# Kernel optimization log

Hardware: AMD Instinct MI355X
Metric: run time of the kernel (lower is better)

## Reference

```python
import jax, jax.numpy as jnp
import numpy as np

D_MODEL = 1024
D_STATE = 16
D_CONV = 3
EXPAND = 2
D_INNER = EXPAND * D_MODEL
BATCH = 1
SEQ = 2048


def _xavier(key, fan_in, fan_out, shape):
    lim = float(np.sqrt(6.0 / (fan_in + fan_out)))
    return jax.random.uniform(key, shape, jnp.float32, -lim, lim)


def setup_inputs() -> dict:
    key = jax.random.key(0)
    ks = jax.random.split(key, 8)
    return {
        "x": jax.random.normal(ks[0], (BATCH, SEQ, D_MODEL), jnp.float32),
        # torch Linear weight (out,in) stored transposed as (in,out) for x @ W
        "in_proj_w": _xavier(ks[1], D_MODEL, 2 * D_INNER, (D_MODEL, 2 * D_INNER)),
        "in_proj_b": jnp.zeros((2 * D_INNER,), jnp.float32),
        "conv_w": _xavier(ks[2], D_MODEL * D_CONV, D_INNER, (D_INNER, D_MODEL, D_CONV)),
        "conv_b": jax.random.normal(ks[3], (D_INNER,), jnp.float32) * 0.02,
        # A_log shifted negative so softplus(A_log) is tiny and the (unstable-by-construction)
        # recurrence with A_bar=exp(+A*dt)>1 stays finite over SEQ steps
        "A_log": jax.random.normal(ks[4], (D_INNER, D_STATE), jnp.float32) * 0.1 - 6.0,
        "D": jnp.ones((D_INNER,), jnp.float32),
        "x_proj_w": _xavier(ks[5], D_INNER, 2 * D_STATE, (D_INNER, 2 * D_STATE)),
        "x_proj_b": jnp.zeros((2 * D_STATE,), jnp.float32),
        "gate_w": _xavier(ks[6], D_INNER, D_INNER, (D_INNER, D_INNER)),
        "gate_b": jnp.zeros((D_INNER,), jnp.float32),
        "o_proj_w": _xavier(ks[7], D_INNER, D_MODEL, (D_INNER, D_MODEL)),
        "o_proj_b": jnp.zeros((D_MODEL,), jnp.float32),
    }


def _forward(x, in_proj_w, in_proj_b, conv_w, conv_b, A_log, D, x_proj_w, x_proj_b,
             gate_w, gate_b, o_proj_w, o_proj_b):
    B, S, _ = x.shape
    # causal depthful conv: torch pads both sides by d_conv-1 then truncates to S,
    # which equals left-pad-only by d_conv-1
    xc = jax.lax.conv_general_dilated(
        x.transpose(0, 2, 1), conv_w, (1,), [(D_CONV - 1, 0)],
        dimension_numbers=("NCH", "OIH", "NCH"))
    x_conv = xc.transpose(0, 2, 1) + conv_b            # (B,S,d_inner)

    xz = x @ in_proj_w + in_proj_b                      # (B,S,2*d_inner)
    z = xz[..., D_INNER:]                               # gate branch (x_inner unused)

    A = jax.nn.softplus(A_log)                          # (d_inner,d_state)
    bc = x_conv @ x_proj_w + x_proj_b                   # (B,S,2*d_state)
    Bm, Cm = bc[..., :D_STATE], bc[..., D_STATE:]
    dt = jax.nn.sigmoid(jnp.mean(x_conv, axis=-1, keepdims=True)) + 0.001  # (B,S,1)
    gate = jax.nn.sigmoid(x_conv @ gate_w + gate_b)
    u = x_conv * gate                                   # (B,S,d_inner)

    dtE = dt[..., None]                                 # (B,S,1,1)
    A_bar = jnp.exp(A[None, None] * dtE)                # (B,S,d_inner,d_state)
    B_bar = A_bar * Bm[:, :, None, :] * dtE             # (B,S,d_inner,d_state)

    def step(h, inp):
        ab, bb, ut, ct = inp                            # (B,di,ds),(B,di,ds),(B,di),(B,ds)
        h = ab * h + bb * ut[:, :, None]
        y = jnp.einsum("bds,bs->bd", h, ct) + D * ut
        return h, y

    h0 = jnp.zeros((B, D_INNER, D_STATE), x.dtype)
    _, ys = jax.lax.scan(
        step, h0,
        (A_bar.transpose(1, 0, 2, 3), B_bar.transpose(1, 0, 2, 3),
         u.transpose(1, 0, 2), Cm.transpose(1, 0, 2)))
    out = ys.transpose(1, 0, 2) * jax.nn.sigmoid(z)     # (B,S,d_inner)
    return out @ o_proj_w + o_proj_b                    # (B,S,d_model)


def reference(x, in_proj_w, in_proj_b, conv_w, conv_b, A_log, D, x_proj_w, x_proj_b,
              gate_w, gate_b, o_proj_w, o_proj_b):
    return _forward(x, in_proj_w, in_proj_b, conv_w, conv_b, A_log, D,
                    x_proj_w, x_proj_b, gate_w, gate_b, o_proj_w, o_proj_b)
```

## Files before the change

kernel.cpp:

```cpp
#include <hip/hip_runtime.h>
#include <hip/hip_bf16.h>
#include <math.h>

typedef __attribute__((ext_vector_type(8))) short short8;
typedef __attribute__((ext_vector_type(4))) float f32x4;

#define NCH 128
#define CT 16

__device__ __forceinline__ unsigned short f2bf(float f) {
  unsigned u = __builtin_bit_cast(unsigned, f);
  u += 0x7fffu + ((u >> 16) & 1u);
  return (unsigned short)(u >> 16);
}
__device__ __forceinline__ float bf2f(unsigned short u) {
  return __builtin_bit_cast(float, (unsigned)u << 16);
}
__device__ __forceinline__ float sigm(float x) { return 1.f / (1.f + __expf(-x)); }
__device__ __forceinline__ float exps(float x) {
  return 1.f + x * (1.f + x * (0.5f + x * 0.16666667f));
}

__device__ __forceinline__ void stage16(const void* g, void* l) {
  __builtin_amdgcn_global_load_lds(
      (const __attribute__((address_space(1))) unsigned int*)(unsigned long long)g,
      (__attribute__((address_space(3))) unsigned int*)(unsigned)(unsigned long long)l,
      16, 0, 0);
}

__global__ __launch_bounds__(256) void prep_uber(
    const float* __restrict__ x, const float* __restrict__ conv_w,
    const float* __restrict__ A_log, const float* __restrict__ in_proj_w,
    const float* __restrict__ gate_w, const float* __restrict__ o_proj_w,
    unsigned short* __restrict__ xb, unsigned short* __restrict__ cwt,
    float* __restrict__ cAb, unsigned short* __restrict__ wzt,
    unsigned short* __restrict__ gwt, unsigned short* __restrict__ owt) {
  __shared__ float tile[32][33];
  int bx = blockIdx.x;
  if (bx < 2050) {
    int idx = (bx * 256 + threadIdx.x) * 4;
    if (idx >= 2050 * 1024) return;
    int row = idx >> 10, col = idx & 1023;
    float v0 = 0.f, v1 = 0.f, v2 = 0.f, v3 = 0.f;
    if (row >= 2) {
      const float4 v = *(const float4*)(x + (size_t)(row - 2) * 1024 + col);
      v0 = v.x; v1 = v.y; v2 = v.z; v3 = v.w;
    }
    unsigned long long pk = (unsigned long long)f2bf(v0)
        | ((unsigned long long)f2bf(v1) << 16)
        | ((unsigned long long)f2bf(v2) << 32)
        | ((unsigned long long)f2bf(v3) << 48);
    *(unsigned long long*)(xb + idx) = pk;
    return;
  }
  bx -= 2050;
  if (bx < 8192) {
    int idx = bx * 256 + threadIdx.x;
    int d = idx >> 10, i = idx & 1023;
    const float* p = conv_w + (size_t)d * 3072 + (size_t)i * 3;
    unsigned short* q = cwt + (size_t)d * 3072 + i;
    q[0] = f2bf(p[0]);
    q[1024] = f2bf(p[1]);
    q[2048] = f2bf(p[2]);
    return;
  }
  bx -= 8192;
  if (bx < 128) {
    int i = bx * 256 + threadIdx.x;
    cAb[i] = log1pf(__expf(A_log[i]));
    return;
  }
  bx -= 128;
  const float* W;
  unsigned short* Wt;
  int src_ld, col_off, rowsI, n0, i0;
  if (bx < 2048) {
    W = in_proj_w; Wt = wzt; src_ld = 4096; col_off = 2048; rowsI = 1024;
    n0 = (bx & 63) * 32; i0 = (bx >> 6) * 32;
  } else if (bx < 2048 + 4096) {
    int b = bx - 2048;
    W = gate_w; Wt = gwt; src_ld = 2048; col_off = 0; rowsI = 2048;
    n0 = (b & 63) * 32; i0 = (b >> 6) * 32;
  } else {
    int b = bx - 2048 - 4096;
    W = o_proj_w; Wt = owt; src_ld = 1024; col_off = 0; rowsI = 2048;
    n0 = (b & 31) * 32; i0 = (b >> 5) * 32;
  }
  int tx = threadIdx.x & 31, ty = threadIdx.x >> 5;
#pragma unroll
  for (int rr = 0; rr < 32; rr += 8)
    tile[ty + rr][tx] = W[(size_t)(i0 + ty + rr) * src_ld + col_off + n0 + tx];
  __syncthreads();
#pragma unroll
  for (int rr = 0; rr < 32; rr += 8)
    Wt[(size_t)(n0 + ty + rr) * rowsI + i0 + tx] = f2bf(tile[tx][ty + rr]);
}

template <int MODE>
__device__ __forceinline__ void gemm_sq_body(
    const unsigned short* __restrict__ A, int lda,
    const unsigned short* __restrict__ Bt, int ldb, int K,
    const float* __restrict__ bias,
    float* __restrict__ outf, int ldo,
    unsigned short* __restrict__ outb,
    int bm, int bn,
    unsigned short (*As)[128 * 64], unsigned short (*Bs)[128 * 64]) {
  const int tid = threadIdx.x;
  const int lane = tid & 63;
  const int w = tid >> 6;
  const int wr = w >> 1, wc = w & 1;

  f32x4 acc[4][4];
#pragma unroll
  for (int m = 0; m < 4; ++m)
#pragma unroll
    for (int n = 0; n < 4; ++n)
#pragma unroll
      for (int j = 0; j < 4; ++j) acc[m][n][j] = 0.f;

  const int srow = lane >> 3;
  const int sslot = (lane & 7) ^ srow;
  const unsigned short* Ab = A + (size_t)(bm * 128 + srow) * lda + sslot * 8;
  const unsigned short* Bb = Bt + (size_t)(bn * 128 + srow) * ldb + sslot * 8;

  const int r = lane & 15;
  const int g = lane >> 4;
  const int nk = K >> 6;

  auto stage = [&](int buf, int k0) {
#pragma unroll
    for (int i = 0; i < 4; ++i) {
      const int cb = w * 4 + i;
      stage16(Ab + (size_t)(cb * 8) * lda + k0, &As[buf][cb * 512]);
    }
#pragma unroll
    for (int i = 0; i < 4; ++i) {
      const int cb = w * 4 + i;
      stage16(Bb + (size_t)(cb * 8) * ldb + k0, &Bs[buf][cb * 512]);
    }
  };

  auto compute = [&](int buf) {
#pragma unroll
    for (int kk = 0; kk < 64; kk += 32) {
      const int sb = (kk >> 3) + g;
      short8 af[4], bfr[4];
#pragma unroll
      for (int m = 0; m < 4; ++m) {
        const int R = wr * 64 + m * 16 + r;
        af[m] = *(const short8*)&As[buf][R * 64 + ((sb ^ (R & 7)) << 3)];
      }
#pragma unroll
      for (int n = 0; n < 4; ++n) {
        const int R = wc * 64 + n * 16 + r;
        bfr[n] = *(const short8*)&Bs[buf][R * 64 + ((sb ^ (R & 7)) << 3)];
      }
#pragma unroll
      for (int m = 0; m < 4; ++m)
#pragma unroll
        for (int n = 0; n < 4; ++n)
          acc[m][n] = __builtin_amdgcn_mfma_f32_16x16x32_bf16(af[m], bfr[n], acc[m][n], 0, 0, 0);
    }
  };

  stage(0, 0);
  int cur = 0;
  for (int kt = 0; kt < nk; ++kt) {
    if (kt + 1 < nk) {
      stage(cur ^ 1, (kt + 1) * 64);
      asm volatile("s_waitcnt vmcnt(8)" ::: "memory");
    } else {
      asm volatile("s_waitcnt vmcnt(0)" ::: "memory");
    }
    __builtin_amdgcn_s_barrier();
    __builtin_amdgcn_sched_barrier(0);
    compute(cur);
    __builtin_amdgcn_s_barrier();
    cur ^= 1;
  }

  const int cc = lane & 15;
  const int cr = g * 4;
#pragma unroll
  for (int m = 0; m < 4; ++m) {
#pragma unroll
    for (int n = 0; n < 4; ++n) {
      const int col = bn * 128 + wc * 64 + n * 16 + cc;
      const float bv = bias[col];
#pragma unroll
      for (int j = 0; j < 4; ++j) {
        const int row = bm * 128 + wr * 64 + m * 16 + cr + j;
        const size_t o = (size_t)row * ldo + col;
        float v = acc[m][n][j] + bv;
        if (MODE == 0) { outb[o] = f2bf(v); }
        else if (MODE == 1) { outf[o] = v; }
        else { outb[o] = f2bf(sigm(v)); }
      }
    }
  }
}

__global__ __launch_bounds__(256, 2) void gemm_convz(
    const unsigned short* __restrict__ xb,
    const unsigned short* __restrict__ cwt,
    const unsigned short* __restrict__ wzt,
    const float* __restrict__ conv_b,
    const float* __restrict__ z_b,
    unsigned short* __restrict__ xcb,
    unsigned short* __restrict__ zpre_b) {
  __shared__ unsigned short As[2][128 * 64];
  __shared__ unsigned short Bs[2][128 * 64];
  const bool isz = blockIdx.y >= 16;
  gemm_sq_body<0>(isz ? xb + 2048 : xb, 1024,
                  isz ? wzt : cwt, isz ? 1024 : 3072, isz ? 1024 : 3072,
                  isz ? z_b : conv_b, nullptr, 2048,
                  isz ? zpre_b : xcb,
                  blockIdx.x, isz ? blockIdx.y - 16 : blockIdx.y, As, Bs);
}

#define RB 4
__global__ __launch_bounds__(256, 2) void gemm_gate64_bcdt(
    const unsigned short* __restrict__ xcb,
    const unsigned short* __restrict__ gwt,
    const float* __restrict__ gate_b,
    unsigned short* __restrict__ gpre_b,
    const float* __restrict__ xpw, const float* __restrict__ xpb,
    float* __restrict__ Bc, float* __restrict__ Cc, float* __restrict__ dt) {
  constexpr int L = 4;
  __shared__ __attribute__((aligned(16))) char smem[49152];
  unsigned short (*As)[4096] = (unsigned short(*)[4096])smem;
  unsigned short (*Bs)[4096] = (unsigned short(*)[4096])(smem + 24576);
  const int tid = threadIdx.x;
  const int lane = tid & 63;
  const int w = tid >> 6;

  if (blockIdx.y >= 32) {
    float (*row)[2048] = (float(*)[2048])smem;
    float (*pj)[8][32] = (float(*)[8][32])(smem + 32768);
    const int b = (blockIdx.y - 32) * 32 + blockIdx.x;
    const int s0 = b * RB;
    for (int i = tid; i < RB * 256; i += 256) {
      int ri = i >> 8, c8 = i & 255;
      short8 v = *(const short8*)&xcb[(size_t)(s0 + ri) * 2048 + c8 * 8];
#pragma unroll
      for (int j = 0; j < 8; ++j) row[ri][c8 * 8 + j] = bf2f((unsigned short)v[j]);
    }
    __syncthreads();
    {
      float l = 0.f;
      for (int i = lane; i < 2048; i += 64) l += row[w][i];
#pragma unroll
      for (int off = 32; off > 0; off >>= 1) l += __shfl_down(l, off);
      if (lane == 0) dt[s0 + w] = sigm(l * (1.f / 2048.f)) + 0.001f;
    }
    const int j = tid & 31, seg = tid >> 5;
    float acc[RB] = {0.f, 0.f, 0.f, 0.f};
    const int kbase = seg * 256;
    for (int k = 0; k < 256; ++k) {
      float wv2 = xpw[(size_t)(kbase + k) * 32 + j];
#pragma unroll
      for (int ri = 0; ri < RB; ++ri) acc[ri] += row[ri][kbase + k] * wv2;
    }
#pragma unroll
    for (int ri = 0; ri < RB; ++ri) pj[ri][seg][j] = acc[ri];
    __syncthreads();
    if (tid < 32 * RB) {
      int ri = tid >> 5, jj = tid & 31;
      float v = xpb[jj];
#pragma unroll
      for (int q = 0; q < 8; ++q) v += pj[ri][q][jj];
      if (jj < 16) Bc[(size_t)(s0 + ri) * 16 + jj] = v;
      else Cc[(size_t)(s0 + ri) * 16 + jj - 16] = v;
    }
    return;
  }

  const int wr = w >> 1, wc = w & 1;
  const int bm = blockIdx.x, bn = blockIdx.y;

  f32x4 acc[2][2];
#pragma unroll
  for (int m = 0; m < 2; ++m)
#pragma unroll
    for (int n = 0; n < 2; ++n)
#pragma unroll
      for (int j = 0; j < 4; ++j) acc[m][n][j] = 0.f;

  const int srow = lane >> 3;
  const int sslot = (lane & 7) ^ srow;
  const unsigned short* Ab = xcb + (size_t)(bm * 64 + srow) * 2048 + sslot * 8;
  const unsigned short* Bb = gwt + (size_t)(bn * 64 + srow) * 2048 + sslot * 8;
  const int r = lane & 15;
  const int g = lane >> 4;
  const int nk = 2048 >> 6;

  auto stage = [&](int buf, int k0) {
#pragma unroll
    for (int i = 0; i < 2; ++i) {
      const int cb = w * 2 + i;
      stage16(Ab + (size_t)(cb * 8) * 2048 + k0, &As[buf][cb * 512]);
      stage16(Bb + (size_t)(cb * 8) * 2048 + k0, &Bs[buf][cb * 512]);
    }
  };
  auto compute = [&](int buf) {
#pragma unroll
    for (int kk = 0; kk < 64; kk += 32) {
      const int sb = (kk >> 3) + g;
      short8 af[2], bfr[2];
#pragma unroll
      for (int m = 0; m < 2; ++m) {
        const int R = wr * 32 + m * 16 + r;
        af[m] = *(const short8*)&As[buf][R * 64 + ((sb ^ (R & 7)) << 3)];
      }
#pragma unroll
      for (int n = 0; n < 2; ++n) {
        const int R = wc * 32 + n * 16 + r;
        bfr[n] = *(const short8*)&Bs[buf][R * 64 + ((sb ^ (R & 7)) << 3)];
      }
#pragma unroll
      for (int m = 0; m < 2; ++m)
#pragma unroll
        for (int n = 0; n < 2; ++n)
          acc[m][n] = __builtin_amdgcn_mfma_f32_16x16x32_bf16(af[m], bfr[n], acc[m][n], 0, 0, 0);
    }
  };

  stage(0, 0);
  stage(1, 64);
  int cur = 0, nxt = 2;
  for (int kt = 0; kt < nk; ++kt) {
    if (kt + 2 < nk) {
      stage(nxt, (kt + 2) * 64);
      asm volatile("s_waitcnt vmcnt(%c0)" ::"i"(2 * L) : "memory");
    } else if (kt + 1 < nk) {
      asm volatile("s_waitcnt vmcnt(%c0)" ::"i"(L) : "memory");
    } else {
      asm volatile("s_waitcnt vmcnt(0)" ::: "memory");
    }
    __builtin_amdgcn_s_barrier();
    __builtin_amdgcn_sched_barrier(0);
    compute(cur);
    __builtin_amdgcn_s_barrier();
    cur = (cur == 2) ? 0 : cur + 1;
    nxt = (nxt == 2) ? 0 : nxt + 1;
  }

  const int cc = lane & 15;
  const int cr = g * 4;
#pragma unroll
  for (int m = 0; m < 2; ++m)
#pragma unroll
    for (int n = 0; n < 2; ++n) {
      const int col = bn * 64 + wc * 32 + n * 16 + cc;
      const float bv = gate_b[col];
#pragma unroll
      for (int j = 0; j < 4; ++j) {
        const int row = bm * 64 + wr * 32 + m * 16 + cr + j;
        gpre_b[(size_t)row * 2048 + col] = f2bf(sigm(acc[m][n][j] + bv));
      }
    }
}

__global__ __launch_bounds__(256, 2) void gemm_out(
    const unsigned short* __restrict__ A, int lda,
    const unsigned short* __restrict__ Bt, int ldb, int K,
    const float* __restrict__ bias,
    float* __restrict__ outf, int ldo) {
  constexpr int L = 4;
  __shared__ unsigned short As[3][64 * 64];
  __shared__ unsigned short Bs[3][64 * 64];
  const int tid = threadIdx.x;
  const int lane = tid & 63;
  const int w = tid >> 6;
  const int wr = w >> 1, wc = w & 1;
  const int bm = blockIdx.x, bn = blockIdx.y;

  f32x4 acc[2][2];
#pragma unroll
  for (int m = 0; m < 2; ++m)
#pragma unroll
    for (int n = 0; n < 2; ++n)
#pragma unroll
      for (int j = 0; j < 4; ++j) acc[m][n][j] = 0.f;

  const int srow = lane >> 3;
  const int sslot = (lane & 7) ^ srow;
  const unsigned short* Ab = A + (size_t)(bm * 64 + srow) * lda + sslot * 8;
  const unsigned short* Bb = Bt + (size_t)(bn * 64 + srow) * ldb + sslot * 8;
  const int r = lane & 15;
  const int g = lane >> 4;
  const int nk = K >> 6;

  auto stage = [&](int buf, int k0) {
#pragma unroll
    for (int i = 0; i < 2; ++i) {
      const int cb = w * 2 + i;
      stage16(Ab + (size_t)(cb * 8) * lda + k0, &As[buf][cb * 512]);
      stage16(Bb + (size_t)(cb * 8) * ldb + k0, &Bs[buf][cb * 512]);
    }
  };
  auto compute = [&](int buf) {
#pragma unroll
    for (int kk = 0; kk < 64; kk += 32) {
      const int sb = (kk >> 3) + g;
      short8 af[2], bfr[2];
#pragma unroll
      for (int m = 0; m < 2; ++m) {
        const int R = wr * 32 + m * 16 + r;
        af[m] = *(const short8*)&As[buf][R * 64 + ((sb ^ (R & 7)) << 3)];
      }
#pragma unroll
      for (int n = 0; n < 2; ++n) {
        const int R = wc * 32 + n * 16 + r;
        bfr[n] = *(const short8*)&Bs[buf][R * 64 + ((sb ^ (R & 7)) << 3)];
      }
#pragma unroll
      for (int m = 0; m < 2; ++m)
#pragma unroll
        for (int n = 0; n < 2; ++n)
          acc[m][n] = __builtin_amdgcn_mfma_f32_16x16x32_bf16(af[m], bfr[n], acc[m][n], 0, 0, 0);
    }
  };

  stage(0, 0);
  stage(1, 64);
  int cur = 0, nxt = 2;
  for (int kt = 0; kt < nk; ++kt) {
    if (kt + 2 < nk) {
      stage(nxt, (kt + 2) * 64);
      asm volatile("s_waitcnt vmcnt(%c0)" ::"i"(2 * L) : "memory");
    } else if (kt + 1 < nk) {
      asm volatile("s_waitcnt vmcnt(%c0)" ::"i"(L) : "memory");
    } else {
      asm volatile("s_waitcnt vmcnt(0)" ::: "memory");
    }
    __builtin_amdgcn_s_barrier();
    __builtin_amdgcn_sched_barrier(0);
    compute(cur);
    __builtin_amdgcn_s_barrier();
    cur = (cur == 2) ? 0 : cur + 1;
    nxt = (nxt == 2) ? 0 : nxt + 1;
  }

  const int cc = lane & 15;
  const int cr = g * 4;
#pragma unroll
  for (int m = 0; m < 2; ++m)
#pragma unroll
    for (int n = 0; n < 2; ++n) {
      const int col = bn * 64 + wc * 32 + n * 16 + cc;
      const float bv = bias[col];
#pragma unroll
      for (int j = 0; j < 4; ++j) {
        const int row = bm * 64 + wr * 32 + m * 16 + cr + j;
        outf[(size_t)row * ldo + col] = acc[m][n][j] + bv;
      }
    }
}

__global__ __launch_bounds__(256) void scan_local(const float* __restrict__ cAb,
                                                  const float* __restrict__ dt,
                                                  const float* __restrict__ Bc,
                                                  const float* __restrict__ Cc,
                                                  const unsigned short* __restrict__ xcb,
                                                  const unsigned short* __restrict__ gpre,
                                                  const float* __restrict__ Dp,
                                                  unsigned short* __restrict__ yloc,
                                                  unsigned short* __restrict__ Hend) {
  const int d0 = blockIdx.x * 256;
  const int d = d0 + threadIdx.x;
  const int c = blockIdx.y;
  __shared__ float sU[CT][256];
  __shared__ float sB[CT][16], sC[CT][16], sdt[CT];
  for (int i = threadIdx.x; i < CT * 32; i += 256) {
    int t = i >> 5, c8 = i & 31;
    size_t base = (size_t)(c * CT + t) * 2048 + d0 + c8 * 8;
    short8 vx = *(const short8*)&xcb[base];
    short8 vg = *(const short8*)&gpre[base];
#pragma unroll
    for (int j = 0; j < 8; ++j)
      sU[t][c8 * 8 + j] = bf2f((unsigned short)vx[j]) * bf2f((unsigned short)vg[j]);
  }
  for (int i = threadIdx.x; i < CT * 16; i += 256) {
    sB[i >> 4][i & 15] = Bc[(size_t)c * CT * 16 + i];
    sC[i >> 4][i & 15] = Cc[(size_t)c * CT * 16 + i];
  }
  if (threadIdx.x < CT) sdt[threadIdx.x] = dt[c * CT + threadIdx.x];
  __syncthreads();
  float cA[16], h[16];
#pragma unroll
  for (int n = 0; n < 16; ++n) {
    cA[n] = cAb[(size_t)d * 16 + n];
    h[n] = 0.f;
  }
  const float Dv = Dp[d];
  for (int t = 0; t < CT; ++t) {
    const float dtv = sdt[t];
    const float uv = sU[t][threadIdx.x];
    const float du = dtv * uv;
    float y = Dv * uv;
#pragma unroll
    for (int n = 0; n < 16; ++n) {
      float ab = exps(cA[n] * dtv);
      h[n] = ab * (h[n] + sB[t][n] * du);
      y += h[n] * sC[t][n];
    }
    yloc[(size_t)(c * CT + t) * 2048 + d] = f2bf(y);
  }
#pragma unroll
  for (int n = 0; n < 16; ++n) Hend[(size_t)c * 32768 + (size_t)d * 16 + n] = f2bf(h[n]);
}

__global__ __launch_bounds__(256) void scan_carry(const float* __restrict__ cAb,
                                                  const float* __restrict__ dt,
                                                  unsigned short* H) {
  const int g = blockIdx.x * 256 + threadIdx.x;
  __shared__ float sdt[2048];
  __shared__ float sS[NCH];
  for (int i = threadIdx.x; i < 2048; i += 256) sdt[i] = dt[i];
  __syncthreads();
  if (threadIdx.x < NCH) {
    float s = 0.f;
#pragma unroll
    for (int t = 0; t < CT; ++t) s += sdt[threadIdx.x * CT + t];
    sS[threadIdx.x] = s;
  }
  __syncthreads();
  const float cA = cAb[g];
  float h = 0.f;
  for (int cb = 0; cb < NCH; cb += 16) {
    float hl[16];
#pragma unroll
    for (int i = 0; i < 16; ++i) hl[i] = bf2f(H[(size_t)(cb + i) * 32768 + g]);
#pragma unroll
    for (int i = 0; i < 16; ++i) {
      H[(size_t)(cb + i) * 32768 + g] = f2bf(h);
      h = exps(cA * sS[cb + i]) * h + hl[i];
    }
  }
}

__global__ __launch_bounds__(256) void scan_final(const float* __restrict__ cAb,
                                                  const float* __restrict__ dt,
                                                  const float* __restrict__ Cc,
                                                  const unsigned short* __restrict__ yloc,
                                                  const unsigned short* __restrict__ zpre,
                                                  const unsigned short* __restrict__ H,
                                                  unsigned short* __restrict__ ob) {
  const int d = blockIdx.x * 256 + threadIdx.x;
  const int c = blockIdx.y;
  __shared__ float sC[CT][16], sT[CT], sdt[CT];
  for (int i = threadIdx.x; i < CT * 16; i += 256) sC[i >> 4][i & 15] = Cc[(size_t)c * CT * 16 + i];
  if (threadIdx.x < CT) sdt[threadIdx.x] = dt[c * CT + threadIdx.x];
  __syncthreads();
  if (threadIdx.x < CT) {
    float a = 0.f;
    for (int t = 0; t <= threadIdx.x; ++t) a += sdt[t];
    sT[threadIdx.x] = a;
  }
  __syncthreads();
  float cA[16], h0[16];
#pragma unroll
  for (int n = 0; n < 16; ++n) {
    cA[n] = cAb[(size_t)d * 16 + n];
    h0[n] = bf2f(H[(size_t)c * 32768 + (size_t)d * 16 + n]);
  }
  for (int t = 0; t < CT; ++t) {
    const size_t idx = (size_t)(c * CT + t) * 2048 + d;
    const float Tt = sT[t];
    float y = bf2f(yloc[idx]);
#pragma unroll
    for (int n = 0; n < 16; ++n) y += sC[t][n] * exps(cA[n] * Tt) * h0[n];
    ob[idx] = f2bf(y * sigm(bf2f(zpre[idx])));
  }
}

extern "C" void kernel_launch(void* const* d_in, const int* in_sizes, int n_in,
                              void* d_out, int out_size, void* d_ws, size_t ws_size,
                              hipStream_t stream) {
  (void)in_sizes; (void)n_in; (void)out_size; (void)ws_size;
  const float* x = (const float*)d_in[0];
  const float* in_proj_w = (const float*)d_in[1];
  const float* in_proj_b = (const float*)d_in[2];
  const float* conv_w = (const float*)d_in[3];
  const float* conv_b = (const float*)d_in[4];
  const float* A_log = (const float*)d_in[5];
  const float* Dp = (const float*)d_in[6];
  const float* x_proj_w = (const float*)d_in[7];
  const float* x_proj_b = (const float*)d_in[8];
  const float* gate_w = (const float*)d_in[9];
  const float* gate_b = (const float*)d_in[10];
  const float* o_proj_w = (const float*)d_in[11];
  const float* o_proj_b = (const float*)d_in[12];

  char* ws = (char*)d_ws;
  size_t off = 0;
  unsigned short* xb = (unsigned short*)(ws + off); off += (size_t)2050 * 1024 * 2;
  off = (off + 255) & ~(size_t)255;
  unsigned short* cwt = (unsigned short*)(ws + off); off += (size_t)2048 * 3072 * 2;
  unsigned short* wzt = (unsigned short*)(ws + off); off += (size_t)2048 * 1024 * 2;
  unsigned short* gwt = (unsigned short*)(ws + off); off += (size_t)2048 * 2048 * 2;
  unsigned short* owt = (unsigned short*)(ws + off); off += (size_t)1024 * 2048 * 2;
  unsigned short* xcb = (unsigned short*)(ws + off); off += (size_t)2048 * 2048 * 2;
  unsigned short* zpre_b = (unsigned short*)(ws + off); off += (size_t)2048 * 2048 * 2;
  unsigned short* gpre_b = (unsigned short*)(ws + off); off += (size_t)2048 * 2048 * 2;
  unsigned short* yloc = (unsigned short*)(ws + off); off += (size_t)2048 * 2048 * 2;
  float* dtv = (float*)(ws + off); off += (size_t)2048 * 4;
  float* Bc = (float*)(ws + off); off += (size_t)2048 * 16 * 4;
  float* Cc = (float*)(ws + off); off += (size_t)2048 * 16 * 4;
  float* cAb = (float*)(ws + off); off += (size_t)32768 * 4;
  unsigned short* H = (unsigned short*)(ws + off); off += (size_t)NCH * 32768 * 2;
  unsigned short* ob = yloc;

  prep_uber<<<18562, 256, 0, stream>>>(x, conv_w, A_log, in_proj_w, gate_w, o_proj_w,
                                       xb, cwt, cAb, wzt, gwt, owt);

  gemm_convz<<<dim3(16, 32), 256, 0, stream>>>(xb, cwt, wzt, conv_b, in_proj_b + 2048, xcb, zpre_b);

  gemm_gate64_bcdt<<<dim3(32, 48), 256, 0, stream>>>(xcb, gwt, gate_b, gpre_b,
                                                     x_proj_w, x_proj_b, Bc, Cc, dtv);

  scan_local<<<dim3(8, NCH), 256, 0, stream>>>(cAb, dtv, Bc, Cc, xcb, gpre_b, Dp, yloc, H);
  scan_carry<<<128, 256, 0, stream>>>(cAb, dtv, H);
  scan_final<<<dim3(8, NCH), 256, 0, stream>>>(cAb, dtv, Cc, yloc, zpre_b, H, ob);

  gemm_out<<<dim3(32, 16), 256, 0, stream>>>(ob, 2048, owt, 2048, 2048, o_proj_b, (float*)d_out, 1024);
}
```

Measured before the change: 152.0 us.

## Switch GEMMs to 128x64 tiles, raise occupancy, and swizzle block order

```diff
diff --git a/kernel.cpp b/kernel.cpp
--- a/kernel.cpp
+++ b/kernel.cpp
@@ -97,31 +97,35 @@
 }
 
 template <int MODE>
-__device__ __forceinline__ void gemm_sq_body(
+__device__ __forceinline__ void gemm_rect_body(
     const unsigned short* __restrict__ A, int lda,
     const unsigned short* __restrict__ Bt, int ldb, int K,
     const float* __restrict__ bias,
     float* __restrict__ outf, int ldo,
     unsigned short* __restrict__ outb,
-    int bm, int bn,
-    unsigned short (*As)[128 * 64], unsigned short (*Bs)[128 * 64]) {
+    int bm, int bn, char* smem) {
+  constexpr int BM = 128, BN = 64;
+  constexpr int IA = 4, IB = 2, L = IA + IB;
+  unsigned short (*As)[BM * 64] = (unsigned short(*)[BM * 64])smem;
+  unsigned short (*Bs)[BN * 64] = (unsigned short(*)[BN * 64])(smem + 32768);
+
   const int tid = threadIdx.x;
   const int lane = tid & 63;
   const int w = tid >> 6;
   const int wr = w >> 1, wc = w & 1;
 
-  f32x4 acc[4][4];
+  f32x4 acc[4][2];
 #pragma unroll
   for (int m = 0; m < 4; ++m)
 #pragma unroll
-    for (int n = 0; n < 4; ++n)
+    for (int n = 0; n < 2; ++n)
 #pragma unroll
       for (int j = 0; j < 4; ++j) acc[m][n][j] = 0.f;
 
   const int srow = lane >> 3;
   const int sslot = (lane & 7) ^ srow;
-  const unsigned short* Ab = A + (size_t)(bm * 128 + srow) * lda + sslot * 8;
-  const unsigned short* Bb = Bt + (size_t)(bn * 128 + srow) * ldb + sslot * 8;
+  const unsigned short* Ab = A + (size_t)(bm * BM + srow) * lda + sslot * 8;
+  const unsigned short* Bb = Bt + (size_t)(bn * BN + srow) * ldb + sslot * 8;
 
   const int r = lane & 15;
   const int g = lane >> 4;
@@ -129,13 +133,13 @@
 
   auto stage = [&](int buf, int k0) {
 #pragma unroll
-    for (int i = 0; i < 4; ++i) {
-      const int cb = w * 4 + i;
+    for (int i = 0; i < IA; ++i) {
+      const int cb = w * IA + i;
       stage16(Ab + (size_t)(cb * 8) * lda + k0, &As[buf][cb * 512]);
     }
 #pragma unroll
-    for (int i = 0; i < 4; ++i) {
-      const int cb = w * 4 + i;
+    for (int i = 0; i < IB; ++i) {
+      const int cb = w * IB + i;
       stage16(Bb + (size_t)(cb * 8) * ldb + k0, &Bs[buf][cb * 512]);
     }
   };
@@ -144,21 +148,21 @@
 #pragma unroll
     for (int kk = 0; kk < 64; kk += 32) {
       const int sb = (kk >> 3) + g;
-      short8 af[4], bfr[4];
+      short8 af[4], bfr[2];
 #pragma unroll
       for (int m = 0; m < 4; ++m) {
         const int R = wr * 64 + m * 16 + r;
         af[m] = *(const short8*)&As[buf][R * 64 + ((sb ^ (R & 7)) << 3)];
       }
 #pragma unroll
-      for (int n = 0; n < 4; ++n) {
-        const int R = wc * 64 + n * 16 + r;
+      for (int n = 0; n < 2; ++n) {
+        const int R = wc * 32 + n * 16 + r;
         bfr[n] = *(const short8*)&Bs[buf][R * 64 + ((sb ^ (R & 7)) << 3)];
       }
 #pragma unroll
       for (int m = 0; m < 4; ++m)
 #pragma unroll
-        for (int n = 0; n < 4; ++n)
+        for (int n = 0; n < 2; ++n)
           acc[m][n] = __builtin_amdgcn_mfma_f32_16x16x32_bf16(af[m], bfr[n], acc[m][n], 0, 0, 0);
     }
   };
@@ -168,7 +172,7 @@
   for (int kt = 0; kt < nk; ++kt) {
     if (kt + 1 < nk) {
       stage(cur ^ 1, (kt + 1) * 64);
-      asm volatile("s_waitcnt vmcnt(8)" ::: "memory");
+      asm volatile("s_waitcnt vmcnt(%c0)" ::"i"(L) : "memory");
     } else {
       asm volatile("s_waitcnt vmcnt(0)" ::: "memory");
     }
@@ -184,12 +188,12 @@
 #pragma unroll
   for (int m = 0; m < 4; ++m) {
 #pragma unroll
-    for (int n = 0; n < 4; ++n) {
-      const int col = bn * 128 + wc * 64 + n * 16 + cc;
+    for (int n = 0; n < 2; ++n) {
+      const int col = bn * BN + wc * 32 + n * 16 + cc;
       const float bv = bias[col];
 #pragma unroll
       for (int j = 0; j < 4; ++j) {
-        const int row = bm * 128 + wr * 64 + m * 16 + cr + j;
+        const int row = bm * BM + wr * 64 + m * 16 + cr + j;
         const size_t o = (size_t)row * ldo + col;
         float v = acc[m][n][j] + bv;
         if (MODE == 0) { outb[o] = f2bf(v); }
@@ -200,7 +204,7 @@
   }
 }
 
-__global__ __launch_bounds__(256, 2) void gemm_convz(
+__global__ __launch_bounds__(256, 3) void gemm_convz(
     const unsigned short* __restrict__ xb,
     const unsigned short* __restrict__ cwt,
     const unsigned short* __restrict__ wzt,
@@ -208,28 +212,28 @@
     const float* __restrict__ z_b,
     unsigned short* __restrict__ xcb,
     unsigned short* __restrict__ zpre_b) {
-  __shared__ unsigned short As[2][128 * 64];
-  __shared__ unsigned short Bs[2][128 * 64];
-  const bool isz = blockIdx.y >= 16;
-  gemm_sq_body<0>(isz ? xb + 2048 : xb, 1024,
-                  isz ? wzt : cwt, isz ? 1024 : 3072, isz ? 1024 : 3072,
-                  isz ? z_b : conv_b, nullptr, 2048,
-                  isz ? zpre_b : xcb,
-                  blockIdx.x, isz ? blockIdx.y - 16 : blockIdx.y, As, Bs);
+  __shared__ __attribute__((aligned(16))) char smem[49152];
+  const int id = blockIdx.x + blockIdx.y * 16;
+  const int logical = (id & 7) * 128 + (id >> 3);
+  const int bm = logical & 15;
+  const int ly = logical >> 4;
+  const bool isz = ly >= 32;
+  gemm_rect_body<0>(isz ? xb + 2048 : xb, 1024,
+                    isz ? wzt : cwt, isz ? 1024 : 3072, isz ? 1024 : 3072,
+                    isz ? z_b : conv_b, nullptr, 2048,
+                    isz ? zpre_b : xcb,
+                    bm, isz ? ly - 32 : ly, smem);
 }
 
 #define RB 4
-__global__ __launch_bounds__(256, 2) void gemm_gate64_bcdt(
+__global__ __launch_bounds__(256, 3) void gemm_gate_bcdt(
     const unsigned short* __restrict__ xcb,
     const unsigned short* __restrict__ gwt,
     const float* __restrict__ gate_b,
     unsigned short* __restrict__ gpre_b,
     const float* __restrict__ xpw, const float* __restrict__ xpb,
     float* __restrict__ Bc, float* __restrict__ Cc, float* __restrict__ dt) {
-  constexpr int L = 4;
   __shared__ __attribute__((aligned(16))) char smem[49152];
-  unsigned short (*As)[4096] = (unsigned short(*)[4096])smem;
-  unsigned short (*Bs)[4096] = (unsigned short(*)[4096])(smem + 24576);
   const int tid = threadIdx.x;
   const int lane = tid & 63;
   const int w = tid >> 6;
@@ -237,7 +241,7 @@
   if (blockIdx.y >= 32) {
     float (*row)[2048] = (float(*)[2048])smem;
     float (*pj)[8][32] = (float(*)[8][32])(smem + 32768);
-    const int b = (blockIdx.y - 32) * 32 + blockIdx.x;
+    const int b = (blockIdx.y - 32) * 16 + blockIdx.x;
     const int s0 = b * RB;
     for (int i = tid; i < RB * 256; i += 256) {
       int ri = i >> 8, c8 = i & 255;
@@ -275,90 +279,8 @@
     return;
   }
 
-  const int wr = w >> 1, wc = w & 1;
-  const int bm = blockIdx.x, bn = blockIdx.y;
-
-  f32x4 acc[2][2];
-#pragma unroll
-  for (int m = 0; m < 2; ++m)
-#pragma unroll
-    for (int n = 0; n < 2; ++n)
-#pragma unroll
-      for (int j = 0; j < 4; ++j) acc[m][n][j] = 0.f;
-
-  const int srow = lane >> 3;
-  const int sslot = (lane & 7) ^ srow;
-  const unsigned short* Ab = xcb + (size_t)(bm * 64 + srow) * 2048 + sslot * 8;
-  const unsigned short* Bb = gwt + (size_t)(bn * 64 + srow) * 2048 + sslot * 8;
-  const int r = lane & 15;
-  const int g = lane >> 4;
-  const int nk = 2048 >> 6;
-
-  auto stage = [&](int buf, int k0) {
-#pragma unroll
-    for (int i = 0; i < 2; ++i) {
-      const int cb = w * 2 + i;
-      stage16(Ab + (size_t)(cb * 8) * 2048 + k0, &As[buf][cb * 512]);
-      stage16(Bb + (size_t)(cb * 8) * 2048 + k0, &Bs[buf][cb * 512]);
-    }
-  };
-  auto compute = [&](int buf) {
-#pragma unroll
-    for (int kk = 0; kk < 64; kk += 32) {
-      const int sb = (kk >> 3) + g;
-      short8 af[2], bfr[2];
-#pragma unroll
-      for (int m = 0; m < 2; ++m) {
-        const int R = wr * 32 + m * 16 + r;
-        af[m] = *(const short8*)&As[buf][R * 64 + ((sb ^ (R & 7)) << 3)];
-      }
-#pragma unroll
-      for (int n = 0; n < 2; ++n) {
-        const int R = wc * 32 + n * 16 + r;
-        bfr[n] = *(const short8*)&Bs[buf][R * 64 + ((sb ^ (R & 7)) << 3)];
-      }
-#pragma unroll
-      for (int m = 0; m < 2; ++m)
-#pragma unroll
-        for (int n = 0; n < 2; ++n)
-          acc[m][n] = __builtin_amdgcn_mfma_f32_16x16x32_bf16(af[m], bfr[n], acc[m][n], 0, 0, 0);
-    }
-  };
-
-  stage(0, 0);
-  stage(1, 64);
-  int cur = 0, nxt = 2;
-  for (int kt = 0; kt < nk; ++kt) {
-    if (kt + 2 < nk) {
-      stage(nxt, (kt + 2) * 64);
-      asm volatile("s_waitcnt vmcnt(%c0)" ::"i"(2 * L) : "memory");
-    } else if (kt + 1 < nk) {
-      asm volatile("s_waitcnt vmcnt(%c0)" ::"i"(L) : "memory");
-    } else {
-      asm volatile("s_waitcnt vmcnt(0)" ::: "memory");
-    }
-    __builtin_amdgcn_s_barrier();
-    __builtin_amdgcn_sched_barrier(0);
-    compute(cur);
-    __builtin_amdgcn_s_barrier();
-    cur = (cur == 2) ? 0 : cur + 1;
-    nxt = (nxt == 2) ? 0 : nxt + 1;
-  }
-
-  const int cc = lane & 15;
-  const int cr = g * 4;
-#pragma unroll
-  for (int m = 0; m < 2; ++m)
-#pragma unroll
-    for (int n = 0; n < 2; ++n) {
-      const int col = bn * 64 + wc * 32 + n * 16 + cc;
-      const float bv = gate_b[col];
-#pragma unroll
-      for (int j = 0; j < 4; ++j) {
-        const int row = bm * 64 + wr * 32 + m * 16 + cr + j;
-        gpre_b[(size_t)row * 2048 + col] = f2bf(sigm(acc[m][n][j] + bv));
-      }
-    }
+  gemm_rect_body<3>(xcb, 2048, gwt, 2048, 2048, gate_b, nullptr, 2048, gpre_b,
+                    blockIdx.x, blockIdx.y, smem);
 }
 
 __global__ __launch_bounds__(256, 2) void gemm_out(
@@ -373,7 +295,9 @@
   const int lane = tid & 63;
   const int w = tid >> 6;
   const int wr = w >> 1, wc = w & 1;
-  const int bm = blockIdx.x, bn = blockIdx.y;
+  const int id = blockIdx.x + blockIdx.y * 32;
+  const int logical = (id & 7) * 64 + (id >> 3);
+  const int bm = logical & 31, bn = logical >> 5;
 
   f32x4 acc[2][2];
 #pragma unroll
@@ -615,10 +539,10 @@
   prep_uber<<<18562, 256, 0, stream>>>(x, conv_w, A_log, in_proj_w, gate_w, o_proj_w,
                                        xb, cwt, cAb, wzt, gwt, owt);
 
-  gemm_convz<<<dim3(16, 32), 256, 0, stream>>>(xb, cwt, wzt, conv_b, in_proj_b + 2048, xcb, zpre_b);
-
-  gemm_gate64_bcdt<<<dim3(32, 48), 256, 0, stream>>>(xcb, gwt, gate_b, gpre_b,
-                                                     x_proj_w, x_proj_b, Bc, Cc, dtv);
+  gemm_convz<<<dim3(16, 64), 256, 0, stream>>>(xb, cwt, wzt, conv_b, in_proj_b + 2048, xcb, zpre_b);
+
+  gemm_gate_bcdt<<<dim3(16, 64), 256, 0, stream>>>(xcb, gwt, gate_b, gpre_b,
+                                                   x_proj_w, x_proj_b, Bc, Cc, dtv);
 
   scan_local<<<dim3(8, NCH), 256, 0, stream>>>(cAb, dtv, Bc, Cc, xcb, gpre_b, Dp, yloc, H);
   scan_carry<<<128, 256, 0, stream>>>(cAb, dtv, H);
```

New measurement: 173.4 us. 1.14x slower.
